# Kernel optimization log

Measured on AMD Instinct MI355X. Metric: run time of the kernel, lower is better.

## Reference

```python
import jax, jax.numpy as jnp
from jax import lax
import numpy as np

SEQ_LEN, BATCH, X_DIM = 512, 128, 256
PHI, R, OUT = 512, 256, 256
ALPHAS = (0.0, 0.5, 0.9, 0.99)
MU = PHI * len(ALPHAS)


def setup_inputs() -> dict:
    key = jax.random.key(0)
    ks = jax.random.split(key, 4)
    s = 0.02  # xavier-ish scale for stability
    return {
        "inputs": jax.random.normal(ks[0], (SEQ_LEN, BATCH, X_DIM), jnp.float32),
        "W_mu2r": jax.random.normal(ks[1], (R, MU), jnp.float32) * s,
        "b_mu2r": jnp.zeros((R,), jnp.float32),
        "W_xr2phi": jax.random.normal(ks[2], (PHI, X_DIM + R), jnp.float32) * s,
        "b_xr2phi": jnp.zeros((PHI,), jnp.float32),
        "W_mu2o": jax.random.normal(ks[3], (OUT, MU), jnp.float32) * s,
        "b_mu2o": jnp.zeros((OUT,), jnp.float32),
    }


def reference(inputs, W_mu2r, b_mu2r, W_xr2phi, b_xr2phi, W_mu2o, b_mu2o):
    A = jnp.asarray(ALPHAS, dtype=inputs.dtype)          # (n_alpha,) non-trainable buffer
    n_alpha = A.shape[0]
    phi_size = W_xr2phi.shape[0]
    # A_mask = kron(A, ones(1, phi)) -> each alpha repeated phi_size times: (1, mu)
    a_mask = jnp.repeat(A, phi_size)[None, :]

    def step(mu, x):
        r = jax.nn.relu(mu @ W_mu2r.T + b_mu2r)                             # (B, r)
        phi = jax.nn.relu(jnp.concatenate([x, r], axis=1) @ W_xr2phi.T + b_xr2phi)  # (B, phi)
        phi_tile = jnp.tile(phi, (1, n_alpha))                              # kron(ones, phi): (B, mu)
        mu = a_mask * mu + (1.0 - a_mask) * phi_tile
        return mu, None

    mu0 = jnp.zeros((inputs.shape[1], phi_size * n_alpha), inputs.dtype)
    mu, _ = lax.scan(step, mu0, inputs)
    return jax.nn.relu(mu @ W_mu2o.T + b_mu2o)  # (B, out)
```

## Files before the change

### kernel.cpp

```cpp
#include <hip/hip_runtime.h>
#include <hip/hip_bf16.h>

#define SEQ   512
#define BATCH 128
#define XD    256
#define PHID  512
#define RD    256
#define OUTD  256
#define NPHI  8
#define NS    16
#define NO    16
#define NBLK  (NPHI + NS + NO)
#define RING  16

typedef __attribute__((ext_vector_type(8))) short short8;
typedef __attribute__((ext_vector_type(4))) float floatx4;

#define MFMA(a, b, c) __builtin_amdgcn_mfma_f32_16x16x32_bf16((a), (b), (c), 0, 0, 0)

#define WAITVM(N) do { asm volatile("s_waitcnt vmcnt(" #N ")" ::: "memory"); \
                       __builtin_amdgcn_sched_barrier(0); } while (0)

__device__ inline short8 ldg8(const __hip_bfloat16* p) {
    return *reinterpret_cast<const short8*>(p);
}
__device__ inline void ldcc(short8& d, const __hip_bfloat16* p) {
    asm volatile("global_load_dwordx4 %0, %1, off sc1"
                 : "=v"(d) : "v"(p) : "memory");
}
__device__ inline void stcc16(__hip_bfloat16* p, __hip_bfloat16 v) {
    const short sv = __builtin_bit_cast(short, v);
    asm volatile("global_store_short %0, %1, off sc1"
                 :: "v"(p), "v"(sv) : "memory");
}
__device__ inline int flagld(const int* p) {
    return __hip_atomic_load(p, __ATOMIC_RELAXED, __HIP_MEMORY_SCOPE_AGENT);
}
__device__ inline void flag_sc1(int* p, int v) {
    asm volatile("global_store_dword %0, %1, off sc1"
                 :: "v"(p), "v"(v) : "memory");
}

__global__ void convert_x(const float* __restrict__ x, __hip_bfloat16* __restrict__ xbf) {
    const int gid = blockIdx.x * blockDim.x + threadIdx.x;
    const float4 v = reinterpret_cast<const float4*>(x)[gid];
    __hip_bfloat16* d = xbf + 4 * (size_t)gid;
    d[0] = __float2bfloat16(v.x); d[1] = __float2bfloat16(v.y);
    d[2] = __float2bfloat16(v.z); d[3] = __float2bfloat16(v.w);
}

__global__ void __launch_bounds__(256) sru_pipe(
    const float* __restrict__ W1, const float* __restrict__ W2,
    const float* __restrict__ Wo,
    const float* __restrict__ b1, const float* __restrict__ b2,
    const float* __restrict__ bo,
    const __hip_bfloat16* __restrict__ xbf,
    __hip_bfloat16* __restrict__ rbf,
    __hip_bfloat16* __restrict__ phib,
    float* __restrict__ out, int* __restrict__ ctrl)
{
    __shared__ __hip_bfloat16 wlds[32768];
    const int bid  = blockIdx.x;
    const int tid  = threadIdx.x;
    const int wave = tid >> 6;
    const int lane = tid & 63;
    const int quad = lane >> 4;
    const int lrow = lane & 15;
    const int m0   = wave * 32;
    int* rfl = ctrl;
    int* pfl = ctrl + 1024;
    int* ofl = ctrl + 1536;

    if (bid < NPHI) {
        const int j0 = bid * 64;
        for (int i = tid * 4; i < 64 * 512; i += 1024) {
            const int n = i >> 9, k = i & 511;
            const int part = k >> 8, kk = k & 255;
            const float4 v = *reinterpret_cast<const float4*>(&W2[(j0 + n) * 512 + k]);
            __hip_bfloat16* dst = &wlds[(((part * 32 + (kk >> 3)) * 64 + n) << 3) + (kk & 7)];
            dst[0] = __float2bfloat16(v.x); dst[1] = __float2bfloat16(v.y);
            dst[2] = __float2bfloat16(v.z); dst[3] = __float2bfloat16(v.w);
        }
        __syncthreads();
        float bj[4];
        #pragma unroll
        for (int j2 = 0; j2 < 4; ++j2) bj[j2] = b2[j0 + j2 * 16 + lrow];
        const __hip_bfloat16* rb0 = rbf + (m0 + lrow) * RD + 8 * quad;
        const __hip_bfloat16* rb1 = rbf + (m0 + 16 + lrow) * RD + 8 * quad;
        #pragma unroll 1
        for (int t = 0; t < SEQ; ++t) {
            floatx4 acc[2][4] = {};
            const __hip_bfloat16* xt = xbf + (size_t)(t * BATCH + m0) * XD;
            #pragma unroll
            for (int k = 0; k < XD; k += 32) {
                const short8 a0 = ldg8(xt + lrow * XD + k + 8 * quad);
                const short8 a1 = ldg8(xt + (16 + lrow) * XD + k + 8 * quad);
                #pragma unroll
                for (int j2 = 0; j2 < 4; ++j2) {
                    const short8 b = *reinterpret_cast<const short8*>(
                        &wlds[((((k >> 3) + quad) * 64 + j2 * 16 + lrow) << 3)]);
                    acc[0][j2] = MFMA(a0, b, acc[0][j2]);
                    acc[1][j2] = MFMA(a1, b, acc[1][j2]);
                }
            }
            {
                int guard = 0;
                while (true) {
                    bool nr = false;
                    if (lane < 16)      nr = flagld(&rfl[(lane * 4 + wave) * 16]) < t + 1;
                    else if (lane < 32) nr = flagld(&ofl[((lane - 16) * 4 + wave) * 16]) < t - (RING - 1);
                    if (__ballot(nr) == 0) break;
                    if (++guard > 16384) break;
                }
            }
            short8 ra[2][4][2];
            #pragma unroll
            for (int ki = 0; ki < 4; ++ki) {
                ldcc(ra[0][ki][0], rb0 + ki * 32);
                ldcc(ra[0][ki][1], rb1 + ki * 32);
            }
            #pragma unroll
            for (int g = 0; g < 2; ++g) {
                if (g == 0) {
                    #pragma unroll
                    for (int ki = 0; ki < 4; ++ki) {
                        ldcc(ra[1][ki][0], rb0 + 128 + ki * 32);
                        ldcc(ra[1][ki][1], rb1 + 128 + ki * 32);
                    }
                    WAITVM(8);
                } else {
                    WAITVM(0);
                }
                #pragma unroll
                for (int ki = 0; ki < 4; ++ki) {
                    const int k = g * 128 + ki * 32;
                    #pragma unroll
                    for (int j2 = 0; j2 < 4; ++j2) {
                        const short8 b = *reinterpret_cast<const short8*>(
                            &wlds[(((32 + (k >> 3) + quad) * 64 + j2 * 16 + lrow) << 3)]);
                        acc[0][j2] = MFMA(ra[g][ki][0], b, acc[0][j2]);
                        acc[1][j2] = MFMA(ra[g][ki][1], b, acc[1][j2]);
                    }
                }
            }
            __hip_bfloat16* pb = phib + (size_t)(t & (RING - 1)) * BATCH * PHID;
            #pragma unroll
            for (int h = 0; h < 2; ++h)
                #pragma unroll
                for (int j2 = 0; j2 < 4; ++j2)
                    #pragma unroll
                    for (int i = 0; i < 4; ++i) {
                        const int row = m0 + 16 * h + quad * 4 + i;
                        const float v = acc[h][j2][i] + bj[j2];
                        stcc16(pb + row * PHID + j0 + j2 * 16 + lrow,
                               __float2bfloat16(fmaxf(v, 0.f)));
                    }
            asm volatile("s_waitcnt vmcnt(0)" ::: "memory");
            if (lane == 0) flag_sc1(&pfl[(bid * 4 + wave) * 16], t + 1);
        }
    } else if (bid < NPHI + NS) {
        const int sb = bid - NPHI, j0 = sb * 16;
        for (int i = tid * 4; i < 4 * 16 * 512; i += 1024) {
            const int a = i >> 13, rem = i & 8191;
            const int n = rem >> 9, k = rem & 511;
            const float4 v = *reinterpret_cast<const float4*>(
                &W1[(j0 + n) * 2048 + a * 512 + k]);
            __hip_bfloat16* dst = &wlds[(((a * 64 + (k >> 3)) * 16 + n) << 3) + (k & 7)];
            dst[0] = __float2bfloat16(v.x); dst[1] = __float2bfloat16(v.y);
            dst[2] = __float2bfloat16(v.z); dst[3] = __float2bfloat16(v.w);
        }
        __syncthreads();
        const float bjv = b1[j0 + lrow];
        const float pre[4]  = {0.f, 1.f, 9.f, 99.f};
        const float post[4] = {1.f, 0.5f, 0.1f, 0.01f};
        floatx4 s[4][2] = {};
        #pragma unroll 1
        for (int t = 0; t < SEQ; ++t) {
            #pragma unroll
            for (int h = 0; h < 2; ++h)
                #pragma unroll
                for (int i = 0; i < 4; ++i) {
                    const int row = m0 + 16 * h + quad * 4 + i;
                    const float rv = s[0][h][i] + s[1][h][i] + s[2][h][i] + s[3][h][i] + bjv;
                    stcc16(rbf + row * RD + j0 + lrow, __float2bfloat16(fmaxf(rv, 0.f)));
                }
            asm volatile("s_waitcnt vmcnt(0)" ::: "memory");
            if (lane == 0) flag_sc1(&rfl[(sb * 4 + wave) * 16], t + 1);
            if (t == SEQ - 1) break;
            {
                int guard = 0;
                while (true) {
                    bool nr = false;
                    if (lane < 8) nr = flagld(&pfl[(lane * 4 + wave) * 16]) < t + 1;
                    if (__ballot(nr) == 0) break;
                    if (++guard > 16384) break;
                }
            }
            #pragma unroll
            for (int a = 0; a < 4; ++a)
                #pragma unroll
                for (int h = 0; h < 2; ++h)
                    s[a][h] *= pre[a];
            const __hip_bfloat16* pb = phib + (size_t)(t & (RING - 1)) * BATCH * PHID;
            const __hip_bfloat16* pb0 = pb + (m0 + lrow) * PHID + 8 * quad;
            const __hip_bfloat16* pb1 = pb + (m0 + 16 + lrow) * PHID + 8 * quad;
            short8 fa[2][4][2];
            #pragma unroll
            for (int ki = 0; ki < 4; ++ki) {
                ldcc(fa[0][ki][0], pb0 + ki * 32);
                ldcc(fa[0][ki][1], pb1 + ki * 32);
            }
            #pragma unroll
            for (int g = 0; g < 4; ++g) {
                if (g < 3) {
                    #pragma unroll
                    for (int ki = 0; ki < 4; ++ki) {
                        ldcc(fa[(g + 1) & 1][ki][0], pb0 + (g + 1) * 128 + ki * 32);
                        ldcc(fa[(g + 1) & 1][ki][1], pb1 + (g + 1) * 128 + ki * 32);
                    }
                    WAITVM(8);
                } else {
                    WAITVM(0);
                }
                #pragma unroll
                for (int ki = 0; ki < 4; ++ki) {
                    const int k = g * 128 + ki * 32;
                    #pragma unroll
                    for (int a = 0; a < 4; ++a) {
                        const short8 b = *reinterpret_cast<const short8*>(
                            &wlds[(((a * 64 + (k >> 3) + quad) * 16 + lrow) << 3)]);
                        s[a][0] = MFMA(fa[g & 1][ki][0], b, s[a][0]);
                        s[a][1] = MFMA(fa[g & 1][ki][1], b, s[a][1]);
                    }
                }
            }
            #pragma unroll
            for (int a = 0; a < 4; ++a)
                #pragma unroll
                for (int h = 0; h < 2; ++h)
                    s[a][h] *= post[a];
        }
    } else {
        const int ob = bid - NPHI - NS, j0 = ob * 16;
        for (int i = tid * 4; i < 4 * 16 * 512; i += 1024) {
            const int a = i >> 13, rem = i & 8191;
            const int n = rem >> 9, k = rem & 511;
            const float4 v = *reinterpret_cast<const float4*>(
                &Wo[(j0 + n) * 2048 + a * 512 + k]);
            __hip_bfloat16* dst = &wlds[(((a * 64 + (k >> 3)) * 16 + n) << 3) + (k & 7)];
            dst[0] = __float2bfloat16(v.x); dst[1] = __float2bfloat16(v.y);
            dst[2] = __float2bfloat16(v.z); dst[3] = __float2bfloat16(v.w);
        }
        __syncthreads();
        const float pre[4]  = {0.f, 1.f, 9.f, 99.f};
        const float post[4] = {1.f, 0.5f, 0.1f, 0.01f};
        floatx4 o[4][2] = {};
        #pragma unroll 1
        for (int t = 0; t < SEQ; ++t) {
            {
                int guard = 0;
                while (true) {
                    bool nr = false;
                    if (lane < 8) nr = flagld(&pfl[(lane * 4 + wave) * 16]) < t + 1;
                    if (__ballot(nr) == 0) break;
                    if (++guard > 16384) break;
                }
            }
            #pragma unroll
            for (int a = 0; a < 4; ++a)
                #pragma unroll
                for (int h = 0; h < 2; ++h)
                    o[a][h] *= pre[a];
            const __hip_bfloat16* pb = phib + (size_t)(t & (RING - 1)) * BATCH * PHID;
            const __hip_bfloat16* pb0 = pb + (m0 + lrow) * PHID + 8 * quad;
            const __hip_bfloat16* pb1 = pb + (m0 + 16 + lrow) * PHID + 8 * quad;
            short8 fa[2][4][2];
            #pragma unroll
            for (int ki = 0; ki < 4; ++ki) {
                ldcc(fa[0][ki][0], pb0 + ki * 32);
                ldcc(fa[0][ki][1], pb1 + ki * 32);
            }
            #pragma unroll
            for (int g = 0; g < 4; ++g) {
                if (g < 3) {
                    #pragma unroll
                    for (int ki = 0; ki < 4; ++ki) {
                        ldcc(fa[(g + 1) & 1][ki][0], pb0 + (g + 1) * 128 + ki * 32);
                        ldcc(fa[(g + 1) & 1][ki][1], pb1 + (g + 1) * 128 + ki * 32);
                    }
                    WAITVM(8);
                } else {
                    WAITVM(0);
                }
                #pragma unroll
                for (int ki = 0; ki < 4; ++ki) {
                    const int k = g * 128 + ki * 32;
                    #pragma unroll
                    for (int a = 0; a < 4; ++a) {
                        const short8 b = *reinterpret_cast<const short8*>(
                            &wlds[(((a * 64 + (k >> 3) + quad) * 16 + lrow) << 3)]);
                        o[a][0] = MFMA(fa[g & 1][ki][0], b, o[a][0]);
                        o[a][1] = MFMA(fa[g & 1][ki][1], b, o[a][1]);
                    }
                }
            }
            #pragma unroll
            for (int a = 0; a < 4; ++a)
                #pragma unroll
                for (int h = 0; h < 2; ++h)
                    o[a][h] *= post[a];
            if (lane == 0) flag_sc1(&ofl[(ob * 4 + wave) * 16], t + 1);
        }
        const float bjo = bo[j0 + lrow];
        #pragma unroll
        for (int h = 0; h < 2; ++h)
            #pragma unroll
            for (int i = 0; i < 4; ++i) {
                const int row = m0 + 16 * h + quad * 4 + i;
                const float v = o[0][h][i] + o[1][h][i] + o[2][h][i] + o[3][h][i] + bjo;
                out[row * OUTD + j0 + lrow] = fmaxf(v, 0.f);
            }
    }
}

extern "C" void kernel_launch(void* const* d_in, const int* in_sizes, int n_in,
                              void* d_out, int out_size, void* d_ws, size_t ws_size,
                              hipStream_t stream)
{
    const float* x  = (const float*)d_in[0];
    const float* W1 = (const float*)d_in[1];
    const float* b1 = (const float*)d_in[2];
    const float* W2 = (const float*)d_in[3];
    const float* b2 = (const float*)d_in[4];
    const float* Wo = (const float*)d_in[5];
    const float* bo = (const float*)d_in[6];
    float* out = (float*)d_out;
    char* ws = (char*)d_ws;

    constexpr size_t O_CTRL = 0;
    constexpr size_t O_RBF  = 16384;
    constexpr size_t O_PHI  = O_RBF + (size_t)BATCH * RD * 2;
    constexpr size_t O_X    = O_PHI + (size_t)RING * BATCH * PHID * 2;

    hipMemsetAsync(ws + O_CTRL, 0, 12288, stream);
    convert_x<<<SEQ * BATCH * XD / 4 / 256, 256, 0, stream>>>(
        x, (__hip_bfloat16*)(ws + O_X));
    sru_pipe<<<NBLK, 256, 0, stream>>>(
        W1, W2, Wo, b1, b2, bo,
        (const __hip_bfloat16*)(ws + O_X),
        (__hip_bfloat16*)(ws + O_RBF),
        (__hip_bfloat16*)(ws + O_PHI),
        out, (int*)(ws + O_CTRL));
}
```

Before: 4.219 ms.

## Replace producer flags with per-element timestep tags on r and phi data

```diff
diff --git a/kernel.cpp b/kernel.cpp
--- a/kernel.cpp
+++ b/kernel.cpp
@@ -11,10 +11,11 @@
 #define NS    16
 #define NO    16
 #define NBLK  (NPHI + NS + NO)
-#define RING  16
+#define RING  8
 
 typedef __attribute__((ext_vector_type(8))) short short8;
 typedef __attribute__((ext_vector_type(4))) float floatx4;
+typedef __attribute__((ext_vector_type(4))) unsigned int uint4v;
 
 #define MFMA(a, b, c) __builtin_amdgcn_mfma_f32_16x16x32_bf16((a), (b), (c), 0, 0, 0)
 
@@ -24,21 +25,32 @@
 __device__ inline short8 ldg8(const __hip_bfloat16* p) {
     return *reinterpret_cast<const short8*>(p);
 }
-__device__ inline void ldcc(short8& d, const __hip_bfloat16* p) {
-    asm volatile("global_load_dwordx4 %0, %1, off sc1"
-                 : "=v"(d) : "v"(p) : "memory");
-}
-__device__ inline void stcc16(__hip_bfloat16* p, __hip_bfloat16 v) {
-    const short sv = __builtin_bit_cast(short, v);
-    asm volatile("global_store_short %0, %1, off sc1"
-                 :: "v"(p), "v"(sv) : "memory");
+__device__ inline void ldu4(uint4v& d, const unsigned int* p) {
+    asm volatile("global_load_dwordx4 %0, %1, off sc1" : "=v"(d) : "v"(p) : "memory");
+}
+__device__ inline void stu(unsigned int* p, unsigned int v) {
+    asm volatile("global_store_dword %0, %1, off sc1" :: "v"(p), "v"(v) : "memory");
 }
 __device__ inline int flagld(const int* p) {
     return __hip_atomic_load(p, __ATOMIC_RELAXED, __HIP_MEMORY_SCOPE_AGENT);
 }
 __device__ inline void flag_sc1(int* p, int v) {
-    asm volatile("global_store_dword %0, %1, off sc1"
-                 :: "v"(p), "v"(v) : "memory");
+    asm volatile("global_store_dword %0, %1, off sc1" :: "v"(p), "v"(v) : "memory");
+}
+__device__ inline bool tag4(const uint4v q, unsigned int w) {
+    return ((q[0] >> 16) == w) & ((q[1] >> 16) == w) &
+           ((q[2] >> 16) == w) & ((q[3] >> 16) == w);
+}
+__device__ inline short8 pkt(const uint4v a, const uint4v b) {
+    uint4v r;
+    r[0] = (a[0] & 0xffffu) | (a[1] << 16);
+    r[1] = (a[2] & 0xffffu) | (a[3] << 16);
+    r[2] = (b[0] & 0xffffu) | (b[1] << 16);
+    r[3] = (b[2] & 0xffffu) | (b[3] << 16);
+    return __builtin_bit_cast(short8, r);
+}
+__device__ inline unsigned int bfb(float v) {
+    return (unsigned int)__builtin_bit_cast(unsigned short, __float2bfloat16(v));
 }
 
 __global__ void convert_x(const float* __restrict__ x, __hip_bfloat16* __restrict__ xbf) {
@@ -49,14 +61,38 @@
     d[2] = __float2bfloat16(v.z); d[3] = __float2bfloat16(v.w);
 }
 
+#define S_ISSUE(Q, g) do { _Pragma("unroll") \
+  for (int ki = 0; ki < 4; ++ki) { \
+    ldu4(Q[ki*4+0], p0 + (g)*128 + ki*32); \
+    ldu4(Q[ki*4+1], p0 + (g)*128 + ki*32 + 4); \
+    ldu4(Q[ki*4+2], p1 + (g)*128 + ki*32); \
+    ldu4(Q[ki*4+3], p1 + (g)*128 + ki*32 + 4); } } while (0)
+
+#define S_VALID(Q, g) do { int _gd = 0; \
+  while (true) { bool _ok = true; \
+    _Pragma("unroll") for (int _i = 0; _i < 16; ++_i) _ok &= tag4(Q[_i], want); \
+    if (__ballot(!_ok) == 0) break; \
+    if (++_gd > 4096) break; \
+    S_ISSUE(Q, (g)); WAITVM(0); } } while (0)
+
+#define S_CONS(Q, g) do { _Pragma("unroll") \
+  for (int ki = 0; ki < 4; ++ki) { \
+    const short8 _a0 = pkt(Q[ki*4+0], Q[ki*4+1]); \
+    const short8 _a1 = pkt(Q[ki*4+2], Q[ki*4+3]); \
+    const int _k = (g)*128 + ki*32; \
+    _Pragma("unroll") for (int a = 0; a < 4; ++a) { \
+      const short8 _b = *(const short8*)&wlds[(((a*64 + (_k>>3) + quad)*16 + lrow) << 3)]; \
+      s4[a][0] = MFMA(_a0, _b, s4[a][0]); \
+      s4[a][1] = MFMA(_a1, _b, s4[a][1]); } } } while (0)
+
 __global__ void __launch_bounds__(256) sru_pipe(
     const float* __restrict__ W1, const float* __restrict__ W2,
     const float* __restrict__ Wo,
     const float* __restrict__ b1, const float* __restrict__ b2,
     const float* __restrict__ bo,
     const __hip_bfloat16* __restrict__ xbf,
-    __hip_bfloat16* __restrict__ rbf,
-    __hip_bfloat16* __restrict__ phib,
+    unsigned int* __restrict__ rT,
+    unsigned int* __restrict__ phiT,
     float* __restrict__ out, int* __restrict__ ctrl)
 {
     __shared__ __hip_bfloat16 wlds[32768];
@@ -67,9 +103,7 @@
     const int quad = lane >> 4;
     const int lrow = lane & 15;
     const int m0   = wave * 32;
-    int* rfl = ctrl;
-    int* pfl = ctrl + 1024;
-    int* ofl = ctrl + 1536;
+    int* ofl = ctrl;
 
     if (bid < NPHI) {
         const int j0 = bid * 64;
@@ -85,10 +119,11 @@
         float bj[4];
         #pragma unroll
         for (int j2 = 0; j2 < 4; ++j2) bj[j2] = b2[j0 + j2 * 16 + lrow];
-        const __hip_bfloat16* rb0 = rbf + (m0 + lrow) * RD + 8 * quad;
-        const __hip_bfloat16* rb1 = rbf + (m0 + 16 + lrow) * RD + 8 * quad;
+        const unsigned int* r0 = rT + (m0 + lrow) * RD + quad * 8;
+        const unsigned int* r1 = rT + (m0 + 16 + lrow) * RD + quad * 8;
         #pragma unroll 1
         for (int t = 0; t < SEQ; ++t) {
+            const unsigned int want = t + 1;
             floatx4 acc[2][4] = {};
             const __hip_bfloat16* xt = xbf + (size_t)(t * BATCH + m0) * XD;
             #pragma unroll
@@ -97,53 +132,70 @@
                 const short8 a1 = ldg8(xt + (16 + lrow) * XD + k + 8 * quad);
                 #pragma unroll
                 for (int j2 = 0; j2 < 4; ++j2) {
-                    const short8 b = *reinterpret_cast<const short8*>(
-                        &wlds[((((k >> 3) + quad) * 64 + j2 * 16 + lrow) << 3)]);
+                    const short8 b = *(const short8*)&wlds[((((k >> 3) + quad) * 64 + j2 * 16 + lrow) << 3)];
                     acc[0][j2] = MFMA(a0, b, acc[0][j2]);
                     acc[1][j2] = MFMA(a1, b, acc[1][j2]);
                 }
             }
-            {
-                int guard = 0;
-                while (true) {
-                    bool nr = false;
-                    if (lane < 16)      nr = flagld(&rfl[(lane * 4 + wave) * 16]) < t + 1;
-                    else if (lane < 32) nr = flagld(&ofl[((lane - 16) * 4 + wave) * 16]) < t - (RING - 1);
-                    if (__ballot(nr) == 0) break;
-                    if (++guard > 16384) break;
+            { int guard = 0;
+              while (true) {
+                  const bool nr = (lane < 16) &&
+                      (flagld(&ofl[(lane * 4 + wave) * 16]) < t - (RING - 1));
+                  if (__ballot(nr) == 0) break;
+                  if (++guard > (1 << 15)) break;
+              } }
+            uint4v q[16]; short8 pa[8];
+            #pragma unroll
+            for (int ks = 0; ks < 8; ++ks) { ldu4(q[2*ks], r0 + ks*32); ldu4(q[2*ks+1], r0 + ks*32 + 4); }
+            WAITVM(0);
+            { int gd = 0;
+              while (true) {
+                  bool ok = true;
+                  #pragma unroll
+                  for (int i = 0; i < 16; ++i) ok &= tag4(q[i], want);
+                  if (__ballot(!ok) == 0) break;
+                  if (++gd > 4096) break;
+                  #pragma unroll
+                  for (int ks = 0; ks < 8; ++ks) { ldu4(q[2*ks], r0 + ks*32); ldu4(q[2*ks+1], r0 + ks*32 + 4); }
+                  WAITVM(0);
+              } }
+            #pragma unroll
+            for (int ks = 0; ks < 8; ++ks) pa[ks] = pkt(q[2*ks], q[2*ks+1]);
+            #pragma unroll
+            for (int ks = 0; ks < 8; ++ks) { ldu4(q[2*ks], r1 + ks*32); ldu4(q[2*ks+1], r1 + ks*32 + 4); }
+            #pragma unroll
+            for (int ks = 0; ks < 8; ++ks) {
+                const int k = ks * 32;
+                #pragma unroll
+                for (int j2 = 0; j2 < 4; ++j2) {
+                    const short8 b = *(const short8*)&wlds[(((32 + (k >> 3) + quad) * 64 + j2 * 16 + lrow) << 3)];
+                    acc[0][j2] = MFMA(pa[ks], b, acc[0][j2]);
                 }
             }
-            short8 ra[2][4][2];
-            #pragma unroll
-            for (int ki = 0; ki < 4; ++ki) {
-                ldcc(ra[0][ki][0], rb0 + ki * 32);
-                ldcc(ra[0][ki][1], rb1 + ki * 32);
-            }
-            #pragma unroll
-            for (int g = 0; g < 2; ++g) {
-                if (g == 0) {
-                    #pragma unroll
-                    for (int ki = 0; ki < 4; ++ki) {
-                        ldcc(ra[1][ki][0], rb0 + 128 + ki * 32);
-                        ldcc(ra[1][ki][1], rb1 + 128 + ki * 32);
-                    }
-                    WAITVM(8);
-                } else {
-                    WAITVM(0);
-                }
-                #pragma unroll
-                for (int ki = 0; ki < 4; ++ki) {
-                    const int k = g * 128 + ki * 32;
-                    #pragma unroll
-                    for (int j2 = 0; j2 < 4; ++j2) {
-                        const short8 b = *reinterpret_cast<const short8*>(
-                            &wlds[(((32 + (k >> 3) + quad) * 64 + j2 * 16 + lrow) << 3)]);
-                        acc[0][j2] = MFMA(ra[g][ki][0], b, acc[0][j2]);
-                        acc[1][j2] = MFMA(ra[g][ki][1], b, acc[1][j2]);
-                    }
+            WAITVM(0);
+            { int gd = 0;
+              while (true) {
+                  bool ok = true;
+                  #pragma unroll
+                  for (int i = 0; i < 16; ++i) ok &= tag4(q[i], want);
+                  if (__ballot(!ok) == 0) break;
+                  if (++gd > 4096) break;
+                  #pragma unroll
+                  for (int ks = 0; ks < 8; ++ks) { ldu4(q[2*ks], r1 + ks*32); ldu4(q[2*ks+1], r1 + ks*32 + 4); }
+                  WAITVM(0);
+              } }
+            #pragma unroll
+            for (int ks = 0; ks < 8; ++ks) pa[ks] = pkt(q[2*ks], q[2*ks+1]);
+            #pragma unroll
+            for (int ks = 0; ks < 8; ++ks) {
+                const int k = ks * 32;
+                #pragma unroll
+                for (int j2 = 0; j2 < 4; ++j2) {
+                    const short8 b = *(const short8*)&wlds[(((32 + (k >> 3) + quad) * 64 + j2 * 16 + lrow) << 3)];
+                    acc[1][j2] = MFMA(pa[ks], b, acc[1][j2]);
                 }
             }
-            __hip_bfloat16* pb = phib + (size_t)(t & (RING - 1)) * BATCH * PHID;
+            unsigned int* ps = phiT + (size_t)(t & (RING - 1)) * BATCH * PHID;
             #pragma unroll
             for (int h = 0; h < 2; ++h)
                 #pragma unroll
@@ -152,19 +204,16 @@
                     for (int i = 0; i < 4; ++i) {
                         const int row = m0 + 16 * h + quad * 4 + i;
                         const float v = acc[h][j2][i] + bj[j2];
-                        stcc16(pb + row * PHID + j0 + j2 * 16 + lrow,
-                               __float2bfloat16(fmaxf(v, 0.f)));
+                        stu(ps + row * PHID + j0 + j2 * 16 + lrow,
+                            (want << 16) | bfb(fmaxf(v, 0.f)));
                     }
-            asm volatile("s_waitcnt vmcnt(0)" ::: "memory");
-            if (lane == 0) flag_sc1(&pfl[(bid * 4 + wave) * 16], t + 1);
         }
     } else if (bid < NPHI + NS) {
         const int sb = bid - NPHI, j0 = sb * 16;
         for (int i = tid * 4; i < 4 * 16 * 512; i += 1024) {
             const int a = i >> 13, rem = i & 8191;
             const int n = rem >> 9, k = rem & 511;
-            const float4 v = *reinterpret_cast<const float4*>(
-                &W1[(j0 + n) * 2048 + a * 512 + k]);
+            const float4 v = *reinterpret_cast<const float4*>(&W1[(j0 + n) * 2048 + a * 512 + k]);
             __hip_bfloat16* dst = &wlds[(((a * 64 + (k >> 3)) * 16 + n) << 3) + (k & 7)];
             dst[0] = __float2bfloat16(v.x); dst[1] = __float2bfloat16(v.y);
             dst[2] = __float2bfloat16(v.z); dst[3] = __float2bfloat16(v.w);
@@ -173,80 +222,48 @@
         const float bjv = b1[j0 + lrow];
         const float pre[4]  = {0.f, 1.f, 9.f, 99.f};
         const float post[4] = {1.f, 0.5f, 0.1f, 0.01f};
-        floatx4 s[4][2] = {};
+        floatx4 s4[4][2] = {};
         #pragma unroll 1
         for (int t = 0; t < SEQ; ++t) {
+            const unsigned int want = t + 1;
             #pragma unroll
             for (int h = 0; h < 2; ++h)
                 #pragma unroll
                 for (int i = 0; i < 4; ++i) {
                     const int row = m0 + 16 * h + quad * 4 + i;
-                    const float rv = s[0][h][i] + s[1][h][i] + s[2][h][i] + s[3][h][i] + bjv;
-                    stcc16(rbf + row * RD + j0 + lrow, __float2bfloat16(fmaxf(rv, 0.f)));
+                    const float rv = s4[0][h][i] + s4[1][h][i] + s4[2][h][i] + s4[3][h][i] + bjv;
+                    stu(rT + row * RD + j0 + lrow, (want << 16) | bfb(fmaxf(rv, 0.f)));
                 }
-            asm volatile("s_waitcnt vmcnt(0)" ::: "memory");
-            if (lane == 0) flag_sc1(&rfl[(sb * 4 + wave) * 16], t + 1);
             if (t == SEQ - 1) break;
-            {
-                int guard = 0;
-                while (true) {
-                    bool nr = false;
-                    if (lane < 8) nr = flagld(&pfl[(lane * 4 + wave) * 16]) < t + 1;
-                    if (__ballot(nr) == 0) break;
-                    if (++guard > 16384) break;
-                }
-            }
             #pragma unroll
             for (int a = 0; a < 4; ++a)
                 #pragma unroll
                 for (int h = 0; h < 2; ++h)
-                    s[a][h] *= pre[a];
-            const __hip_bfloat16* pb = phib + (size_t)(t & (RING - 1)) * BATCH * PHID;
-            const __hip_bfloat16* pb0 = pb + (m0 + lrow) * PHID + 8 * quad;
-            const __hip_bfloat16* pb1 = pb + (m0 + 16 + lrow) * PHID + 8 * quad;
-            short8 fa[2][4][2];
-            #pragma unroll
-            for (int ki = 0; ki < 4; ++ki) {
-                ldcc(fa[0][ki][0], pb0 + ki * 32);
-                ldcc(fa[0][ki][1], pb1 + ki * 32);
-            }
-            #pragma unroll
-            for (int g = 0; g < 4; ++g) {
-                if (g < 3) {
-                    #pragma unroll
-                    for (int ki = 0; ki < 4; ++ki) {
-                        ldcc(fa[(g + 1) & 1][ki][0], pb0 + (g + 1) * 128 + ki * 32);
-                        ldcc(fa[(g + 1) & 1][ki][1], pb1 + (g + 1) * 128 + ki * 32);
-                    }
-                    WAITVM(8);
-                } else {
-                    WAITVM(0);
-                }
-                #pragma unroll
-                for (int ki = 0; ki < 4; ++ki) {
-                    const int k = g * 128 + ki * 32;
-                    #pragma unroll
-                    for (int a = 0; a < 4; ++a) {
-                        const short8 b = *reinterpret_cast<const short8*>(
-                            &wlds[(((a * 64 + (k >> 3) + quad) * 16 + lrow) << 3)]);
-                        s[a][0] = MFMA(fa[g & 1][ki][0], b, s[a][0]);
-                        s[a][1] = MFMA(fa[g & 1][ki][1], b, s[a][1]);
-                    }
-                }
-            }
+                    s4[a][h] *= pre[a];
+            const unsigned int* pb = phiT + (size_t)(t & (RING - 1)) * BATCH * PHID;
+            const unsigned int* p0 = pb + (m0 + lrow) * PHID + quad * 8;
+            const unsigned int* p1 = pb + (m0 + 16 + lrow) * PHID + quad * 8;
+            uint4v qa[16], qb[16];
+            S_ISSUE(qa, 0);
+            S_ISSUE(qb, 1);
+            WAITVM(16); S_VALID(qa, 0); S_CONS(qa, 0);
+            S_ISSUE(qa, 2);
+            WAITVM(16); S_VALID(qb, 1); S_CONS(qb, 1);
+            S_ISSUE(qb, 3);
+            WAITVM(16); S_VALID(qa, 2); S_CONS(qa, 2);
+            WAITVM(0);  S_VALID(qb, 3); S_CONS(qb, 3);
             #pragma unroll
             for (int a = 0; a < 4; ++a)
                 #pragma unroll
                 for (int h = 0; h < 2; ++h)
-                    s[a][h] *= post[a];
+                    s4[a][h] *= post[a];
         }
     } else {
         const int ob = bid - NPHI - NS, j0 = ob * 16;
         for (int i = tid * 4; i < 4 * 16 * 512; i += 1024) {
             const int a = i >> 13, rem = i & 8191;
             const int n = rem >> 9, k = rem & 511;
-            const float4 v = *reinterpret_cast<const float4*>(
-                &Wo[(j0 + n) * 2048 + a * 512 + k]);
+            const float4 v = *reinterpret_cast<const float4*>(&Wo[(j0 + n) * 2048 + a * 512 + k]);
             __hip_bfloat16* dst = &wlds[(((a * 64 + (k >> 3)) * 16 + n) << 3) + (k & 7)];
             dst[0] = __float2bfloat16(v.x); dst[1] = __float2bfloat16(v.y);
             dst[2] = __float2bfloat16(v.z); dst[3] = __float2bfloat16(v.w);
@@ -254,61 +271,32 @@
         __syncthreads();
         const float pre[4]  = {0.f, 1.f, 9.f, 99.f};
         const float post[4] = {1.f, 0.5f, 0.1f, 0.01f};
-        floatx4 o[4][2] = {};
+        floatx4 s4[4][2] = {};
         #pragma unroll 1
         for (int t = 0; t < SEQ; ++t) {
-            {
-                int guard = 0;
-                while (true) {
-                    bool nr = false;
-                    if (lane < 8) nr = flagld(&pfl[(lane * 4 + wave) * 16]) < t + 1;
-                    if (__ballot(nr) == 0) break;
-                    if (++guard > 16384) break;
-                }
-            }
+            const unsigned int want = t + 1;
             #pragma unroll
             for (int a = 0; a < 4; ++a)
                 #pragma unroll
                 for (int h = 0; h < 2; ++h)
-                    o[a][h] *= pre[a];
-            const __hip_bfloat16* pb = phib + (size_t)(t & (RING - 1)) * BATCH * PHID;
-            const __hip_bfloat16* pb0 = pb + (m0 + lrow) * PHID + 8 * quad;
-            const __hip_bfloat16* pb1 = pb + (m0 + 16 + lrow) * PHID + 8 * quad;
-            short8 fa[2][4][2];
-            #pragma unroll
-            for (int ki = 0; ki < 4; ++ki) {
-                ldcc(fa[0][ki][0], pb0 + ki * 32);
-                ldcc(fa[0][ki][1], pb1 + ki * 32);
-            }
-            #pragma unroll
-            for (int g = 0; g < 4; ++g) {
-                if (g < 3) {
-                    #pragma unroll
-                    for (int ki = 0; ki < 4; ++ki) {
-                        ldcc(fa[(g + 1) & 1][ki][0], pb0 + (g + 1) * 128 + ki * 32);
-                        ldcc(fa[(g + 1) & 1][ki][1], pb1 + (g + 1) * 128 + ki * 32);
-                    }
-                    WAITVM(8);
-                } else {
-                    WAITVM(0);
-                }
-                #pragma unroll
-                for (int ki = 0; ki < 4; ++ki) {
-                    const int k = g * 128 + ki * 32;
-                    #pragma unroll
-                    for (int a = 0; a < 4; ++a) {
-                        const short8 b = *reinterpret_cast<const short8*>(
-                            &wlds[(((a * 64 + (k >> 3) + quad) * 16 + lrow) << 3)]);
-                        o[a][0] = MFMA(fa[g & 1][ki][0], b, o[a][0]);
-                        o[a][1] = MFMA(fa[g & 1][ki][1], b, o[a][1]);
-                    }
-                }
-            }
+                    s4[a][h] *= pre[a];
+            const unsigned int* pb = phiT + (size_t)(t & (RING - 1)) * BATCH * PHID;
+            const unsigned int* p0 = pb + (m0 + lrow) * PHID + quad * 8;
+            const unsigned int* p1 = pb + (m0 + 16 + lrow) * PHID + quad * 8;
+            uint4v qa[16], qb[16];
+            S_ISSUE(qa, 0);
+            S_ISSUE(qb, 1);
+            WAITVM(16); S_VALID(qa, 0); S_CONS(qa, 0);
+            S_ISSUE(qa, 2);
+            WAITVM(16); S_VALID(qb, 1); S_CONS(qb, 1);
+            S_ISSUE(qb, 3);
+            WAITVM(16); S_VALID(qa, 2); S_CONS(qa, 2);
+            WAITVM(0);  S_VALID(qb, 3); S_CONS(qb, 3);
             #pragma unroll
             for (int a = 0; a < 4; ++a)
                 #pragma unroll
                 for (int h = 0; h < 2; ++h)
-                    o[a][h] *= post[a];
+                    s4[a][h] *= post[a];
             if (lane == 0) flag_sc1(&ofl[(ob * 4 + wave) * 16], t + 1);
         }
         const float bjo = bo[j0 + lrow];
@@ -317,7 +305,7 @@
             #pragma unroll
             for (int i = 0; i < 4; ++i) {
                 const int row = m0 + 16 * h + quad * 4 + i;
-                const float v = o[0][h][i] + o[1][h][i] + o[2][h][i] + o[3][h][i] + bjo;
+                const float v = s4[0][h][i] + s4[1][h][i] + s4[2][h][i] + s4[3][h][i] + bjo;
                 out[row * OUTD + j0 + lrow] = fmaxf(v, 0.f);
             }
     }
@@ -338,17 +326,17 @@
     char* ws = (char*)d_ws;
 
     constexpr size_t O_CTRL = 0;
-    constexpr size_t O_RBF  = 16384;
-    constexpr size_t O_PHI  = O_RBF + (size_t)BATCH * RD * 2;
-    constexpr size_t O_X    = O_PHI + (size_t)RING * BATCH * PHID * 2;
-
-    hipMemsetAsync(ws + O_CTRL, 0, 12288, stream);
+    constexpr size_t O_RT   = 4096;
+    constexpr size_t O_PHIT = O_RT + 131072;
+    constexpr size_t O_X    = O_PHIT + (size_t)RING * BATCH * PHID * 4;
+
+    hipMemsetAsync(ws, 0, O_X, stream);
     convert_x<<<SEQ * BATCH * XD / 4 / 256, 256, 0, stream>>>(
         x, (__hip_bfloat16*)(ws + O_X));
     sru_pipe<<<NBLK, 256, 0, stream>>>(
         W1, W2, Wo, b1, b2, bo,
         (const __hip_bfloat16*)(ws + O_X),
-        (__hip_bfloat16*)(ws + O_RBF),
-        (__hip_bfloat16*)(ws + O_PHI),
+        (unsigned int*)(ws + O_RT),
+        (unsigned int*)(ws + O_PHIT),
         out, (int*)(ws + O_CTRL));
 }
```

After: 8.553 ms. +102.7%, slower.
